# Kernel tuning notes

Measured on AMD Instinct MI355X. Metric: run time of the kernel, lower is better.

Reference implementation:

```python
import jax, jax.numpy as jnp
import numpy as np

V, D, H, L, DFF = 32000, 512, 8, 6, 2048
B, T = 64, 256
PAD_IDX = 1


def _pos_encoding(t, d):
    pos = jnp.arange(t, dtype=jnp.float32)[:, None]          # [t,1]
    i2 = jnp.arange(0, d, 2, dtype=jnp.float32)              # [d/2]
    ang = pos / jnp.power(10000.0, i2 / d)                   # [t,d/2]
    pe = jnp.zeros((t, d), dtype=jnp.float32)
    pe = pe.at[:, 0::2].set(jnp.sin(ang))
    pe = pe.at[:, 1::2].set(jnp.cos(ang))
    return pe


def _ln(x, g, b):
    mu = x.mean(-1, keepdims=True)
    var = ((x - mu) ** 2).mean(-1, keepdims=True)
    return (x - mu) * jax.lax.rsqrt(var + 1e-5) * g + b


def _mha(xq, xkv, Wq, Wk, Wv, Wo, bo, causal):
    b, tq, d = xq.shape
    tk = xkv.shape[1]
    hd = d // H
    q = (xq @ Wq).reshape(b, tq, H, hd)
    k = (xkv @ Wk).reshape(b, tk, H, hd)
    v = (xkv @ Wv).reshape(b, tk, H, hd)
    wei = jnp.einsum('bqhd,bkhd->bhqk', q, k) * (hd ** -0.5)
    if causal:
        mask = jnp.tril(jnp.ones((tq, tk), dtype=bool))
        wei = jnp.where(mask, wei, -jnp.inf)
    wei = jax.nn.softmax(wei, axis=-1)
    out = jnp.einsum('bhqk,bkhd->bqhd', wei, v).reshape(b, tq, d)
    return out @ Wo + bo


def _ffn(x, W1, b1, W2, b2):
    return jax.nn.relu(x @ W1 + b1) @ W2 + b2


def setup_inputs() -> dict:
    key = jax.random.key(0)
    ks = iter(jax.random.split(key, 64))
    nrm = lambda shape: (jax.random.normal(next(ks), shape, dtype=jnp.float32) * 0.02)
    inp = {
        'idx': jax.random.randint(next(ks), (B, T), 0, V),
        'idx_enc': jax.random.randint(next(ks), (B, T), 0, V),
        'targets': jax.random.randint(next(ks), (B, T), 0, V),
        'emb_dec': nrm((V, D)),
        'emb_enc': nrm((V, D)),
        # encoder stacks [L, ...]
        'enc_Wq': nrm((L, D, D)), 'enc_Wk': nrm((L, D, D)), 'enc_Wv': nrm((L, D, D)),
        'enc_Wo': nrm((L, D, D)), 'enc_bo': jnp.zeros((L, D)),
        'enc_ln_g': jnp.ones((L, 2, D)), 'enc_ln_b': jnp.zeros((L, 2, D)),
        'enc_W1': nrm((L, D, DFF)), 'enc_b1': jnp.zeros((L, DFF)),
        'enc_W2': nrm((L, DFF, D)), 'enc_b2': jnp.zeros((L, D)),
        # decoder stacks [L, ...]
        'dec_Wq_sa': nrm((L, D, D)), 'dec_Wk_sa': nrm((L, D, D)), 'dec_Wv_sa': nrm((L, D, D)),
        'dec_Wo_sa': nrm((L, D, D)), 'dec_bo_sa': jnp.zeros((L, D)),
        'dec_Wq_xa': nrm((L, D, D)), 'dec_Wk_xa': nrm((L, D, D)), 'dec_Wv_xa': nrm((L, D, D)),
        'dec_Wo_xa': nrm((L, D, D)), 'dec_bo_xa': jnp.zeros((L, D)),
        'dec_ln_g': jnp.ones((L, 4, D)), 'dec_ln_b': jnp.zeros((L, 4, D)),
        'dec_W1': nrm((L, D, DFF)), 'dec_b1': jnp.zeros((L, DFF)),
        'dec_W2': nrm((L, DFF, D)), 'dec_b2': jnp.zeros((L, D)),
        'lnf_g': jnp.ones((D,)), 'lnf_b': jnp.zeros((D,)),
        'Wlm': nrm((D, V)), 'blm': jnp.zeros((V,)),
    }
    return inp


def reference(idx, idx_enc, targets, emb_dec, emb_enc,
              enc_Wq, enc_Wk, enc_Wv, enc_Wo, enc_bo, enc_ln_g, enc_ln_b,
              enc_W1, enc_b1, enc_W2, enc_b2,
              dec_Wq_sa, dec_Wk_sa, dec_Wv_sa, dec_Wo_sa, dec_bo_sa,
              dec_Wq_xa, dec_Wk_xa, dec_Wv_xa, dec_Wo_xa, dec_bo_xa,
              dec_ln_g, dec_ln_b, dec_W1, dec_b1, dec_W2, dec_b2,
              lnf_g, lnf_b, Wlm, blm):
    t_dec = idx.shape[1]
    t_enc = idx_enc.shape[1]
    pe = _pos_encoding(256, D)
    # encoder
    y = emb_enc[idx_enc] + pe[:t_enc]
    for l in range(L):
        h = _ln(y, enc_ln_g[l, 0], enc_ln_b[l, 0])
        y = y + _mha(h, h, enc_Wq[l], enc_Wk[l], enc_Wv[l], enc_Wo[l], enc_bo[l], causal=False)
        h = _ln(y, enc_ln_g[l, 1], enc_ln_b[l, 1])
        y = y + _ffn(h, enc_W1[l], enc_b1[l], enc_W2[l], enc_b2[l])
    # decoder
    x = emb_dec[idx] + pe[:t_dec]
    for l in range(L):
        h = _ln(x, dec_ln_g[l, 0], dec_ln_b[l, 0])
        x = x + _mha(h, h, dec_Wq_sa[l], dec_Wk_sa[l], dec_Wv_sa[l], dec_Wo_sa[l], dec_bo_sa[l], causal=True)
        hq = _ln(x, dec_ln_g[l, 1], dec_ln_b[l, 1])
        hk = _ln(y, dec_ln_g[l, 2], dec_ln_b[l, 2])
        x = x + _mha(hq, hk, dec_Wq_xa[l], dec_Wk_xa[l], dec_Wv_xa[l], dec_Wo_xa[l], dec_bo_xa[l], causal=False)
        h = _ln(x, dec_ln_g[l, 3], dec_ln_b[l, 3])
        x = x + _ffn(h, dec_W1[l], dec_b1[l], dec_W2[l], dec_b2[l])
    x = _ln(x, lnf_g, lnf_b)
    logits = (x @ Wlm + blm).reshape(-1, V)  # [B*T, V]
    # cross entropy with ignore_index = PAD_IDX, mean over non-ignored
    tgt = targets.reshape(-1)
    logp = jax.nn.log_softmax(logits, axis=-1)
    nll = -jnp.take_along_axis(logp, tgt[:, None], axis=-1)[:, 0]
    valid = (tgt != PAD_IDX).astype(logits.dtype)
    loss = jnp.sum(nll * valid) / jnp.maximum(jnp.sum(valid), 1.0)
    return logits, loss
```

## Files before the change

### kernel.cpp

```cpp
#include <hip/hip_runtime.h>

typedef __attribute__((ext_vector_type(8))) short s8v;
typedef __attribute__((ext_vector_type(4))) float f4v;
using u16 = unsigned short;

__device__ __forceinline__ u16 f2bf(float f) {
  union { float f; unsigned u; } v; v.f = f;
  return (u16)((v.u + 0x7FFFu + ((v.u >> 16) & 1u)) >> 16);
}

__global__ __launch_bounds__(256) void pe_kernel(float* __restrict__ pe) {
  int i = blockIdx.x * 256 + threadIdx.x;
  int t = i >> 8, p = i & 255;
  float ex = (2.f * (float)p) / 512.f;
  float ang = (float)t * expf(-ex * 9.210340371976184f);
  pe[t * 512 + 2 * p]     = sinf(ang);
  pe[t * 512 + 2 * p + 1] = cosf(ang);
}

__global__ __launch_bounds__(256) void wconv_kernel(const float* __restrict__ in,
    u16* __restrict__ out, int R, int C, size_t dstride) {
  __shared__ float tile[64][65];
  const size_t mat = (size_t)R * C;
  const float* src = in + (size_t)blockIdx.z * mat;
  u16* dst = out + (size_t)blockIdx.z * dstride;
  int r0 = blockIdx.x * 64, c0 = blockIdx.y * 64;
  int tr = threadIdx.x >> 6, tc = threadIdx.x & 63;
#pragma unroll
  for (int i = 0; i < 16; ++i)
    tile[i * 4 + tr][tc] = src[(size_t)(r0 + i * 4 + tr) * C + (c0 + tc)];
  __syncthreads();
#pragma unroll
  for (int i = 0; i < 16; ++i)
    dst[(size_t)(c0 + i * 4 + tr) * R + (r0 + tc)] = f2bf(tile[tc][i * 4 + tr]);
}

__global__ __launch_bounds__(256) void embed_kernel(const int* __restrict__ idx,
    const float* __restrict__ emb, const float* __restrict__ pe, float* __restrict__ y) {
  int i = blockIdx.x * 256 + threadIdx.x;
  int row = i >> 7, c = (i & 127) * 4;
  int t = row & 255;
  int tok = idx[row];
  f4v e = *(const f4v*)(emb + (size_t)tok * 512 + c);
  f4v p = *(const f4v*)(pe + (size_t)t * 512 + c);
  *(f4v*)(y + (size_t)row * 512 + c) = e + p;
}

__global__ __launch_bounds__(256) void ln_kernel(const float* __restrict__ x,
    const float* __restrict__ g, const float* __restrict__ b, u16* __restrict__ out) {
  int row = blockIdx.x * 4 + (threadIdx.x >> 6);
  int lane = threadIdx.x & 63;
  const float* xr = x + (size_t)row * 512 + lane * 8;
  f4v v0 = *(const f4v*)xr;
  f4v v1 = *(const f4v*)(xr + 4);
  float s = v0[0] + v0[1] + v0[2] + v0[3] + v1[0] + v1[1] + v1[2] + v1[3];
#pragma unroll
  for (int o = 1; o < 64; o <<= 1) s += __shfl_xor(s, o);
  float mu = s * (1.f / 512.f);
  float q = 0.f;
#pragma unroll
  for (int j = 0; j < 4; ++j) {
    float d0 = v0[j] - mu; q += d0 * d0;
    float d1 = v1[j] - mu; q += d1 * d1;
  }
#pragma unroll
  for (int o = 1; o < 64; o <<= 1) q += __shfl_xor(q, o);
  float rs = rsqrtf(q * (1.f / 512.f) + 1e-5f);
  f4v g0 = *(const f4v*)(g + lane * 8), g1 = *(const f4v*)(g + lane * 8 + 4);
  f4v b0 = *(const f4v*)(b + lane * 8), b1 = *(const f4v*)(b + lane * 8 + 4);
  s8v ov;
#pragma unroll
  for (int j = 0; j < 4; ++j) {
    ov[j]     = (short)f2bf((v0[j] - mu) * rs * g0[j] + b0[j]);
    ov[4 + j] = (short)f2bf((v1[j] - mu) * rs * g1[j] + b1[j]);
  }
  *(s8v*)(out + (size_t)row * 512 + lane * 8) = ov;
}

template<int HAS_BIAS, int ADD_RES, int RELU, int OUT_BF16, int WLOSS, int NT, int SWZM>
__global__ __launch_bounds__(256, 4) void gemm128(
    const u16* __restrict__ A, const u16* __restrict__ Bt,
    const float* __restrict__ bias, const float* __restrict__ res,
    void* __restrict__ outp, int M, int N, int K,
    float* __restrict__ pmax, float* __restrict__ psum) {
  __shared__ __align__(16) u16 smem[2 * 128 * 64];
  u16* As = smem;
  u16* Bs = smem + 128 * 64;
  const int tid = threadIdx.x, lane = tid & 63, w = tid >> 6;
  int bx, by;
  if (SWZM == 1) {
    int flat = blockIdx.y * gridDim.x + blockIdx.x;
    int xcd = flat & 7, local = flat >> 3;
    int p = local / gridDim.y;
    by = local - p * gridDim.y;
    bx = xcd * (gridDim.x >> 3) + p;
  } else {
    int nx = gridDim.x;
    int flat = blockIdx.y * nx + blockIdx.x;
    int per = (nx * gridDim.y) >> 3;
    int sw = (flat & 7) * per + (flat >> 3);
    by = sw / nx; bx = sw - by * nx;
  }
  const int m0 = bx * 128, n0 = by * 128;
  const int wm = (w >> 1) * 64, wn = (w & 1) * 64;
  const int lhi = lane >> 4, llo = lane & 15;
  const int srow = tid >> 3;
  const int sl = tid & 7;
  const int gcol = (sl ^ (srow & 7)) * 8;

  const u16* Ag = A + (size_t)(m0 + srow) * K + gcol;
  const u16* Bg = Bt + (size_t)(n0 + srow) * K + gcol;
  const size_t rstep = (size_t)32 * K;
  const int sx = llo & 7;

  f4v acc[4][4] = {};
  const int nk = K >> 6;
  for (int t = 0; t < nk; ++t) {
    const int kt = t * 64;
#pragma unroll
    for (int q = 0; q < 4; ++q)
      __builtin_amdgcn_global_load_lds(
          (const __attribute__((address_space(1))) void*)(Ag + q * rstep + kt),
          (__attribute__((address_space(3))) void*)(&As[(q * 32 + srow) * 64 + sl * 8]),
          16, 0, 0);
#pragma unroll
    for (int q = 0; q < 4; ++q)
      __builtin_amdgcn_global_load_lds(
          (const __attribute__((address_space(1))) void*)(Bg + q * rstep + kt),
          (__attribute__((address_space(3))) void*)(&Bs[(q * 32 + srow) * 64 + sl * 8]),
          16, 0, 0);
    __syncthreads();
#pragma unroll
    for (int kk = 0; kk < 2; ++kk) {
      s8v af[4], bfv[4];
#pragma unroll
      for (int i = 0; i < 4; ++i)
        af[i] = *(const s8v*)&As[(wm + i * 16 + llo) * 64 + (((kk * 4 + lhi) ^ sx) * 8)];
#pragma unroll
      for (int j = 0; j < 4; ++j)
        bfv[j] = *(const s8v*)&Bs[(wn + j * 16 + llo) * 64 + (((kk * 4 + lhi) ^ sx) * 8)];
#pragma unroll
      for (int i = 0; i < 4; ++i)
#pragma unroll
        for (int j = 0; j < 4; ++j)
          acc[i][j] = __builtin_amdgcn_mfma_f32_16x16x32_bf16(af[i], bfv[j], acc[i][j], 0, 0, 0);
    }
    __syncthreads();
  }

  if (OUT_BF16) {
    float bvj[4];
#pragma unroll
    for (int j = 0; j < 4; ++j)
      bvj[j] = HAS_BIAS ? bias[n0 + wn + j * 16 + llo] : 0.f;
#pragma unroll
    for (int i = 0; i < 4; ++i) {
#pragma unroll
      for (int j = 0; j < 4; ++j) {
        int col = n0 + wn + j * 16 + llo;
#pragma unroll
        for (int r = 0; r < 4; ++r) {
          int row = m0 + wm + i * 16 + lhi * 4 + r;
          float v = acc[i][j][r] + bvj[j];
          if (RELU) v = fmaxf(v, 0.f);
          ((u16*)outp)[(size_t)row * N + col] = f2bf(v);
        }
      }
    }
  } else {
    float* lb = (float*)smem;
    float* wbuf = lb + w * 1088;
    float* lbm = lb + 4608;
    float* lbs = lb + 4864;
    f4v bias4 = {0.f, 0.f, 0.f, 0.f};
    if (HAS_BIAS) bias4 = *(const f4v*)(bias + n0 + wn + llo * 4);
#pragma unroll
    for (int i = 0; i < 4; ++i) {
#pragma unroll
      for (int j = 0; j < 4; ++j)
#pragma unroll
        for (int r = 0; r < 4; ++r)
          wbuf[(lhi * 4 + r) * 68 + j * 16 + llo] = acc[i][j][r];
      asm volatile("s_waitcnt lgkmcnt(0)" ::: "memory");
      __builtin_amdgcn_sched_barrier(0);
#pragma unroll
      for (int p = 0; p < 4; ++p) {
        int r16 = p * 4 + lhi;
        f4v v4 = *(const f4v*)&wbuf[r16 * 68 + llo * 4];
        v4 += bias4;
        int grow = m0 + wm + i * 16 + r16;
        int gcol4 = n0 + wn + llo * 4;
        if (ADD_RES) v4 += *(const f4v*)(res + (size_t)grow * N + gcol4);
        if (RELU) {
          v4[0] = fmaxf(v4[0], 0.f); v4[1] = fmaxf(v4[1], 0.f);
          v4[2] = fmaxf(v4[2], 0.f); v4[3] = fmaxf(v4[3], 0.f);
        }
        float* dst = (float*)outp + (size_t)grow * N + gcol4;
        if (NT) __builtin_nontemporal_store(v4, (f4v*)dst);
        else    *(f4v*)dst = v4;
        if (WLOSS) {
          float mx = fmaxf(fmaxf(v4[0], v4[1]), fmaxf(v4[2], v4[3]));
          mx = fmaxf(mx, __shfl_xor(mx, 1));
          mx = fmaxf(mx, __shfl_xor(mx, 2));
          mx = fmaxf(mx, __shfl_xor(mx, 4));
          mx = fmaxf(mx, __shfl_xor(mx, 8));
          float sum = __expf(v4[0] - mx) + __expf(v4[1] - mx)
                    + __expf(v4[2] - mx) + __expf(v4[3] - mx);
          sum += __shfl_xor(sum, 1); sum += __shfl_xor(sum, 2);
          sum += __shfl_xor(sum, 4); sum += __shfl_xor(sum, 8);
          if (llo == 0) {
            int lr = wm + i * 16 + r16;
            lbm[lr * 2 + (wn >> 6)] = mx;
            lbs[lr * 2 + (wn >> 6)] = sum;
          }
        }
      }
      asm volatile("s_waitcnt lgkmcnt(0)" ::: "memory");
      __builtin_amdgcn_sched_barrier(0);
    }
    if (WLOSS) {
      __syncthreads();
      if (tid < 128) {
        float ma = lbm[tid * 2], mb = lbm[tid * 2 + 1];
        float sa = lbs[tid * 2], sb = lbs[tid * 2 + 1];
        float m = fmaxf(ma, mb);
        float ss = sa * __expf(ma - m) + sb * __expf(mb - m);
        int ntile = N >> 7;
        pmax[(size_t)(m0 + tid) * ntile + by] = m;
        psum[(size_t)(m0 + tid) * ntile + by] = ss;
      }
    }
  }
}

__global__ __launch_bounds__(256) void attn_kernel(
    const u16* __restrict__ Qp, int qs, const u16* __restrict__ Kp,
    const u16* __restrict__ Vp, int kvs, u16* __restrict__ Ob, int causal) {
  __shared__ __align__(16) u16 Ks[256][72];
  __shared__ __align__(16) u16 Vt[64][264];
  __shared__ __align__(16) u16 Ps[4][16][264];
  const int tid = threadIdx.x, lane = tid & 63, w = tid >> 6;
  const int b = blockIdx.x >> 3, h = blockIdx.x & 7;
  const size_t qbase  = (size_t)b * 256 * qs  + (size_t)h * 64;
  const size_t kvbase = (size_t)b * 256 * kvs + (size_t)h * 64;
  const size_t obase  = (size_t)b * 256 * 512 + (size_t)h * 64;
  {
    int t0 = tid >> 3, d0 = (tid & 7) * 8;
#pragma unroll
    for (int it = 0; it < 8; ++it) {
      int t = it * 32 + t0;
      s8v kv = *(const s8v*)(Kp + kvbase + (size_t)t * kvs + d0);
      *(s8v*)&Ks[t][d0] = kv;
      s8v vv = *(const s8v*)(Vp + kvbase + (size_t)t * kvs + d0);
#pragma unroll
      for (int j = 0; j < 8; ++j) Vt[d0 + j][t] = (u16)vv[j];
    }
  }
  __syncthreads();
  const int lhi = lane >> 4, llo = lane & 15;
  for (int qc = 0; qc < 4; ++qc) {
    const int qr0 = w * 64 + qc * 16;
    s8v aq0 = *(const s8v*)(Qp + qbase + (size_t)(qr0 + llo) * qs + lhi * 8);
    s8v aq1 = *(const s8v*)(Qp + qbase + (size_t)(qr0 + llo) * qs + 32 + lhi * 8);
    f4v S[16];
#pragma unroll
    for (int c = 0; c < 16; ++c) {
      s8v bk0 = *(const s8v*)&Ks[c * 16 + llo][lhi * 8];
      s8v bk1 = *(const s8v*)&Ks[c * 16 + llo][32 + lhi * 8];
      f4v z = {0.f, 0.f, 0.f, 0.f};
      z = __builtin_amdgcn_mfma_f32_16x16x32_bf16(aq0, bk0, z, 0, 0, 0);
      S[c] = __builtin_amdgcn_mfma_f32_16x16x32_bf16(aq1, bk1, z, 0, 0, 0);
    }
#pragma unroll
    for (int r = 0; r < 4; ++r) {
      const int tq = qr0 + lhi * 4 + r;
      float mx = -1e30f;
#pragma unroll
      for (int c = 0; c < 16; ++c) {
        float s = S[c][r] * 0.125f;
        if (causal && (c * 16 + llo) > tq) s = -1e30f;
        S[c][r] = s;
        mx = fmaxf(mx, s);
      }
      mx = fmaxf(mx, __shfl_xor(mx, 1));
      mx = fmaxf(mx, __shfl_xor(mx, 2));
      mx = fmaxf(mx, __shfl_xor(mx, 4));
      mx = fmaxf(mx, __shfl_xor(mx, 8));
      float sum = 0.f;
#pragma unroll
      for (int c = 0; c < 16; ++c) { float p = __expf(S[c][r] - mx); S[c][r] = p; sum += p; }
      sum += __shfl_xor(sum, 1); sum += __shfl_xor(sum, 2);
      sum += __shfl_xor(sum, 4); sum += __shfl_xor(sum, 8);
      float inv = 1.f / sum;
#pragma unroll
      for (int c = 0; c < 16; ++c)
        Ps[w][lhi * 4 + r][c * 16 + llo] = f2bf(S[c][r] * inv);
    }
    asm volatile("s_waitcnt lgkmcnt(0)" ::: "memory");
    f4v o[4] = {};
#pragma unroll
    for (int kb = 0; kb < 8; ++kb) {
      s8v pa = *(const s8v*)&Ps[w][llo][kb * 32 + lhi * 8];
#pragma unroll
      for (int nb = 0; nb < 4; ++nb) {
        s8v bv = *(const s8v*)&Vt[nb * 16 + llo][kb * 32 + lhi * 8];
        o[nb] = __builtin_amdgcn_mfma_f32_16x16x32_bf16(pa, bv, o[nb], 0, 0, 0);
      }
    }
#pragma unroll
    for (int nb = 0; nb < 4; ++nb)
#pragma unroll
      for (int r = 0; r < 4; ++r)
        Ob[obase + (size_t)(qr0 + lhi * 4 + r) * 512 + nb * 16 + llo] = f2bf(o[nb][r]);
  }
}

__global__ __launch_bounds__(256) void loss_lse_kernel(const float* __restrict__ pmax,
    const float* __restrict__ psum, const float* __restrict__ logits,
    const int* __restrict__ tgt, float* __restrict__ nll, float* __restrict__ valid) {
  const int w = threadIdx.x >> 6, lane = threadIdx.x & 63;
  const int row = blockIdx.x * 4 + w;
  float m = -1e30f, s = 0.f;
  for (int e = lane; e < 250; e += 64) {
    float pm = pmax[(size_t)row * 250 + e], ps = psum[(size_t)row * 250 + e];
    if (pm > m) { s = s * __expf(m - pm) + ps; m = pm; }
    else          s += ps * __expf(pm - m);
  }
#pragma unroll
  for (int o = 1; o < 64; o <<= 1) {
    float om = __shfl_xor(m, o), os = __shfl_xor(s, o);
    float mm = fmaxf(m, om);
    s = s * __expf(m - mm) + os * __expf(om - mm);
    m = mm;
  }
  if (lane == 0) {
    int t = tgt[row];
    float lse = m + logf(s);
    float v = (t != 1) ? 1.f : 0.f;
    nll[row] = v * (lse - logits[(size_t)row * 32000 + t]);
    valid[row] = v;
  }
}

__global__ __launch_bounds__(256) void loss_final_kernel(const float* __restrict__ nll,
    const float* __restrict__ valid, float* __restrict__ out) {
  __shared__ float sa[256], sb[256];
  int tid = threadIdx.x;
  float s = 0.f, c = 0.f;
  for (int i = tid; i < 16384; i += 256) { s += nll[i]; c += valid[i]; }
  sa[tid] = s; sb[tid] = c;
  __syncthreads();
  for (int st = 128; st > 0; st >>= 1) {
    if (tid < st) { sa[tid] += sa[tid + st]; sb[tid] += sb[tid + st]; }
    __syncthreads();
  }
  if (tid == 0) out[0] = sa[0] / fmaxf(sb[0], 1.f);
}

extern "C" void kernel_launch(void* const* d_in, const int* in_sizes, int n_in,
                              void* d_out, int out_size, void* d_ws, size_t ws_size,
                              hipStream_t stream) {
  (void)in_sizes; (void)n_in; (void)out_size; (void)ws_size;
  const int* idx       = (const int*)d_in[0];
  const int* idx_enc   = (const int*)d_in[1];
  const int* targets   = (const int*)d_in[2];
  const float* emb_dec = (const float*)d_in[3];
  const float* emb_enc = (const float*)d_in[4];
  const float* enc_Wq  = (const float*)d_in[5];
  const float* enc_Wk  = (const float*)d_in[6];
  const float* enc_Wv  = (const float*)d_in[7];
  const float* enc_Wo  = (const float*)d_in[8];
  const float* enc_bo  = (const float*)d_in[9];
  const float* enc_ln_g = (const float*)d_in[10];
  const float* enc_ln_b = (const float*)d_in[11];
  const float* enc_W1  = (const float*)d_in[12];
  const float* enc_b1  = (const float*)d_in[13];
  const float* enc_W2  = (const float*)d_in[14];
  const float* enc_b2  = (const float*)d_in[15];
  const float* dWq_sa  = (const float*)d_in[16];
  const float* dWk_sa  = (const float*)d_in[17];
  const float* dWv_sa  = (const float*)d_in[18];
  const float* dWo_sa  = (const float*)d_in[19];
  const float* dbo_sa  = (const float*)d_in[20];
  const float* dWq_xa  = (const float*)d_in[21];
  const float* dWk_xa  = (const float*)d_in[22];
  const float* dWv_xa  = (const float*)d_in[23];
  const float* dWo_xa  = (const float*)d_in[24];
  const float* dbo_xa  = (const float*)d_in[25];
  const float* dec_ln_g = (const float*)d_in[26];
  const float* dec_ln_b = (const float*)d_in[27];
  const float* dec_W1  = (const float*)d_in[28];
  const float* dec_b1  = (const float*)d_in[29];
  const float* dec_W2  = (const float*)d_in[30];
  const float* dec_b2  = (const float*)d_in[31];
  const float* lnf_g   = (const float*)d_in[32];
  const float* lnf_b   = (const float*)d_in[33];
  const float* Wlm     = (const float*)d_in[34];
  const float* blm     = (const float*)d_in[35];
  float* out_logits = (float*)d_out;
  float* out_loss   = out_logits + (size_t)16384 * 32000;

  size_t off = 0;
  auto alloc = [&](size_t bytes) -> char* {
    char* p = (char*)d_ws + off;
    off += (bytes + 255) & ~(size_t)255;
    return p;
  };
  const size_t SQ = 512 * 512, SF = 512 * 2048;
  u16* tWqkvE = (u16*)alloc(6 * 3 * SQ * 2);
  u16* tWoE   = (u16*)alloc(6 * SQ * 2);
  u16* tW1E   = (u16*)alloc(6 * SF * 2);
  u16* tW2E   = (u16*)alloc(6 * SF * 2);
  u16* tWqkvS = (u16*)alloc(6 * 3 * SQ * 2);
  u16* tWoS   = (u16*)alloc(6 * SQ * 2);
  u16* tWqX   = (u16*)alloc(6 * SQ * 2);
  u16* tWkvX  = (u16*)alloc(6 * 2 * SQ * 2);
  u16* tWoX   = (u16*)alloc(6 * SQ * 2);
  u16* tW1D   = (u16*)alloc(6 * SF * 2);
  u16* tW2D   = (u16*)alloc(6 * SF * 2);
  u16* tWlm   = (u16*)alloc((size_t)32000 * 512 * 2);
  float* pe   = (float*)alloc(256 * 512 * 4);
  float* yE   = (float*)alloc((size_t)16384 * 512 * 4);
  float* xD   = (float*)alloc((size_t)16384 * 512 * 4);
  u16* hA     = (u16*)alloc((size_t)16384 * 512 * 2);
  u16* hB     = (u16*)alloc((size_t)16384 * 512 * 2);
  u16* qkvB   = (u16*)alloc((size_t)16384 * 1536 * 2);
  u16* qB     = (u16*)alloc((size_t)16384 * 512 * 2);
  u16* kvB    = (u16*)alloc((size_t)16384 * 1024 * 2);
  u16* atB    = (u16*)alloc((size_t)16384 * 512 * 2);
  u16* midB   = (u16*)alloc((size_t)16384 * 2048 * 2);
  float* pmax = (float*)alloc((size_t)16384 * 250 * 4);
  float* psum = (float*)alloc((size_t)16384 * 250 * 4);
  float* rnll = (float*)alloc(16384 * 4);
  float* rval = (float*)alloc(16384 * 4);

  dim3 tb(256);
  const size_t S3 = 3 * SQ, S2 = 2 * SQ;
  wconv_kernel<<<dim3(8, 8, 6), tb, 0, stream>>>(enc_Wq, tWqkvE + 0 * SQ, 512, 512, S3);
  wconv_kernel<<<dim3(8, 8, 6), tb, 0, stream>>>(enc_Wk, tWqkvE + 1 * SQ, 512, 512, S3);
  wconv_kernel<<<dim3(8, 8, 6), tb, 0, stream>>>(enc_Wv, tWqkvE + 2 * SQ, 512, 512, S3);
  wconv_kernel<<<dim3(8, 8, 6), tb, 0, stream>>>(enc_Wo, tWoE, 512, 512, SQ);
  wconv_kernel<<<dim3(8, 32, 6), tb, 0, stream>>>(enc_W1, tW1E, 512, 2048, SF);
  wconv_kernel<<<dim3(32, 8, 6), tb, 0, stream>>>(enc_W2, tW2E, 2048, 512, SF);
  wconv_kernel<<<dim3(8, 8, 6), tb, 0, stream>>>(dWq_sa, tWqkvS + 0 * SQ, 512, 512, S3);
  wconv_kernel<<<dim3(8, 8, 6), tb, 0, stream>>>(dWk_sa, tWqkvS + 1 * SQ, 512, 512, S3);
  wconv_kernel<<<dim3(8, 8, 6), tb, 0, stream>>>(dWv_sa, tWqkvS + 2 * SQ, 512, 512, S3);
  wconv_kernel<<<dim3(8, 8, 6), tb, 0, stream>>>(dWo_sa, tWoS, 512, 512, SQ);
  wconv_kernel<<<dim3(8, 8, 6), tb, 0, stream>>>(dWq_xa, tWqX, 512, 512, SQ);
  wconv_kernel<<<dim3(8, 8, 6), tb, 0, stream>>>(dWk_xa, tWkvX + 0 * SQ, 512, 512, S2);
  wconv_kernel<<<dim3(8, 8, 6), tb, 0, stream>>>(dWv_xa, tWkvX + 1 * SQ, 512, 512, S2);
  wconv_kernel<<<dim3(8, 8, 6), tb, 0, stream>>>(dWo_xa, tWoX, 512, 512, SQ);
  wconv_kernel<<<dim3(8, 32, 6), tb, 0, stream>>>(dec_W1, tW1D, 512, 2048, SF);
  wconv_kernel<<<dim3(32, 8, 6), tb, 0, stream>>>(dec_W2, tW2D, 2048, 512, SF);
  wconv_kernel<<<dim3(8, 500, 1), tb, 0, stream>>>(Wlm, tWlm, 512, 32000, (size_t)0);
  pe_kernel<<<256, 256, 0, stream>>>(pe);

  auto ln = [&](const float* xin, const float* g, const float* bb, u16* o) {
    ln_kernel<<<4096, 256, 0, stream>>>(xin, g, bb, o);
  };
  auto g_bf16 = [&](const u16* Ap, const u16* Bp, u16* Op, int N) {
    gemm128<0, 0, 0, 1, 0, 0, 0><<<dim3(128, N / 128), 256, 0, stream>>>(
        Ap, Bp, nullptr, nullptr, Op, 16384, N, 512, nullptr, nullptr);
  };
  auto proj_res = [&](const u16* Ap, const u16* Bp, const float* bi, float* xr, int K) {
    gemm128<1, 1, 0, 0, 0, 0, 0><<<dim3(128, 4), 256, 0, stream>>>(
        Ap, Bp, bi, xr, xr, 16384, 512, K, nullptr, nullptr);
  };
  auto ffn1 = [&](const u16* Ap, const u16* Bp, const float* bi, u16* Op) {
    gemm128<1, 0, 1, 1, 0, 0, 0><<<dim3(128, 16), 256, 0, stream>>>(
        Ap, Bp, bi, nullptr, Op, 16384, 2048, 512, nullptr, nullptr);
  };

  embed_kernel<<<8192, 256, 0, stream>>>(idx_enc, emb_enc, pe, yE);
  for (int l = 0; l < 6; ++l) {
    ln(yE, enc_ln_g + (l * 2 + 0) * 512, enc_ln_b + (l * 2 + 0) * 512, hA);
    g_bf16(hA, tWqkvE + l * S3, qkvB, 1536);
    attn_kernel<<<512, 256, 0, stream>>>(qkvB, 1536, qkvB + 512, qkvB + 1024, 1536, atB, 0);
    proj_res(atB, tWoE + l * SQ, enc_bo + l * 512, yE, 512);
    ln(yE, enc_ln_g + (l * 2 + 1) * 512, enc_ln_b + (l * 2 + 1) * 512, hA);
    ffn1(hA, tW1E + l * SF, enc_b1 + l * 2048, midB);
    proj_res(midB, tW2E + l * SF, enc_b2 + l * 512, yE, 2048);
  }

  embed_kernel<<<8192, 256, 0, stream>>>(idx, emb_dec, pe, xD);
  for (int l = 0; l < 6; ++l) {
    ln(xD, dec_ln_g + (l * 4 + 0) * 512, dec_ln_b + (l * 4 + 0) * 512, hA);
    g_bf16(hA, tWqkvS + l * S3, qkvB, 1536);
    attn_kernel<<<512, 256, 0, stream>>>(qkvB, 1536, qkvB + 512, qkvB + 1024, 1536, atB, 1);
    proj_res(atB, tWoS + l * SQ, dbo_sa + l * 512, xD, 512);
    ln(xD, dec_ln_g + (l * 4 + 1) * 512, dec_ln_b + (l * 4 + 1) * 512, hA);
    ln(yE, dec_ln_g + (l * 4 + 2) * 512, dec_ln_b + (l * 4 + 2) * 512, hB);
    g_bf16(hA, tWqX + l * SQ, qB, 512);
    g_bf16(hB, tWkvX + l * S2, kvB, 1024);
    attn_kernel<<<512, 256, 0, stream>>>(qB, 512, kvB, kvB + 512, 1024, atB, 0);
    proj_res(atB, tWoX + l * SQ, dbo_xa + l * 512, xD, 512);
    ln(xD, dec_ln_g + (l * 4 + 3) * 512, dec_ln_b + (l * 4 + 3) * 512, hA);
    ffn1(hA, tW1D + l * SF, dec_b1 + l * 2048, midB);
    proj_res(midB, tW2D + l * SF, dec_b2 + l * 512, xD, 2048);
  }

  ln(xD, lnf_g, lnf_b, hA);
  gemm128<1, 0, 0, 0, 1, 1, 1><<<dim3(128, 250), 256, 0, stream>>>(
      hA, tWlm, blm, nullptr, out_logits, 16384, 32000, 512, pmax, psum);
  loss_lse_kernel<<<4096, 256, 0, stream>>>(pmax, psum, out_logits, targets, rnll, rval);
  loss_final_kernel<<<1, 256, 0, stream>>>(rnll, rval, out_loss);
}
```

Before: 4.918 ms.

## Rewrite attention as flash-style KV tiling and fuse LN, embedding, cross-attn GEMMs

Attention now walks K/V in four 64-row tiles with an online softmax, keeping Q fragments in registers, skipping fully masked causal tiles, and using much less shared memory so two blocks can share a CU. Embedding is fused with the first layernorm, the two cross-attention layernorms are merged into one launch, and the Q and KV projections run as one dual-operand GEMM launch. The twelve square weight conversions are batched into a single kernel. These cut launches and extra activation passes, but the tiled attention adds more barriers and rescaling work per tile.

Result: no change. 4.836 ms (-1.7%).

```diff
diff --git a/kernel.cpp b/kernel.cpp
--- a/kernel.cpp
+++ b/kernel.cpp
@@ -35,15 +35,47 @@
     dst[(size_t)(c0 + i * 4 + tr) * R + (r0 + tc)] = f2bf(tile[tc][i * 4 + tr]);
 }
 
-__global__ __launch_bounds__(256) void embed_kernel(const int* __restrict__ idx,
-    const float* __restrict__ emb, const float* __restrict__ pe, float* __restrict__ y) {
-  int i = blockIdx.x * 256 + threadIdx.x;
-  int row = i >> 7, c = (i & 127) * 4;
-  int t = row & 255;
-  int tok = idx[row];
-  f4v e = *(const f4v*)(emb + (size_t)tok * 512 + c);
-  f4v p = *(const f4v*)(pe + (size_t)t * 512 + c);
-  *(f4v*)(y + (size_t)row * 512 + c) = e + p;
+struct WcSq { const float* src[12]; u16* dst[12]; unsigned long long dstr[12]; };
+__global__ __launch_bounds__(256) void wconv_sq_kernel(WcSq S) {
+  __shared__ float tile[64][65];
+  int mm = blockIdx.z / 6, l = blockIdx.z % 6;
+  const float* src = S.src[mm] + (size_t)l * 512 * 512;
+  u16* dst = S.dst[mm] + (size_t)l * S.dstr[mm];
+  int r0 = blockIdx.x * 64, c0 = blockIdx.y * 64;
+  int tr = threadIdx.x >> 6, tc = threadIdx.x & 63;
+#pragma unroll
+  for (int i = 0; i < 16; ++i)
+    tile[i * 4 + tr][tc] = src[(size_t)(r0 + i * 4 + tr) * 512 + (c0 + tc)];
+  __syncthreads();
+#pragma unroll
+  for (int i = 0; i < 16; ++i)
+    dst[(size_t)(c0 + i * 4 + tr) * 512 + (r0 + tc)] = f2bf(tile[tc][i * 4 + tr]);
+}
+
+__device__ __forceinline__ void ln_row(f4v v0, f4v v1, const float* g, const float* b,
+                                       int lane, u16* outrow) {
+  float s = v0[0] + v0[1] + v0[2] + v0[3] + v1[0] + v1[1] + v1[2] + v1[3];
+#pragma unroll
+  for (int o = 1; o < 64; o <<= 1) s += __shfl_xor(s, o);
+  float mu = s * (1.f / 512.f);
+  float q = 0.f;
+#pragma unroll
+  for (int j = 0; j < 4; ++j) {
+    float d0 = v0[j] - mu; q += d0 * d0;
+    float d1 = v1[j] - mu; q += d1 * d1;
+  }
+#pragma unroll
+  for (int o = 1; o < 64; o <<= 1) q += __shfl_xor(q, o);
+  float rs = rsqrtf(q * (1.f / 512.f) + 1e-5f);
+  f4v g0 = *(const f4v*)(g + lane * 8), g1 = *(const f4v*)(g + lane * 8 + 4);
+  f4v b0 = *(const f4v*)(b + lane * 8), b1 = *(const f4v*)(b + lane * 8 + 4);
+  s8v ov;
+#pragma unroll
+  for (int j = 0; j < 4; ++j) {
+    ov[j]     = (short)f2bf((v0[j] - mu) * rs * g0[j] + b0[j]);
+    ov[4 + j] = (short)f2bf((v1[j] - mu) * rs * g1[j] + b1[j]);
+  }
+  *(s8v*)(outrow + lane * 8) = ov;
 }
 
 __global__ __launch_bounds__(256) void ln_kernel(const float* __restrict__ x,
@@ -51,38 +83,46 @@
   int row = blockIdx.x * 4 + (threadIdx.x >> 6);
   int lane = threadIdx.x & 63;
   const float* xr = x + (size_t)row * 512 + lane * 8;
-  f4v v0 = *(const f4v*)xr;
-  f4v v1 = *(const f4v*)(xr + 4);
-  float s = v0[0] + v0[1] + v0[2] + v0[3] + v1[0] + v1[1] + v1[2] + v1[3];
-#pragma unroll
-  for (int o = 1; o < 64; o <<= 1) s += __shfl_xor(s, o);
-  float mu = s * (1.f / 512.f);
-  float q = 0.f;
-#pragma unroll
-  for (int j = 0; j < 4; ++j) {
-    float d0 = v0[j] - mu; q += d0 * d0;
-    float d1 = v1[j] - mu; q += d1 * d1;
-  }
-#pragma unroll
-  for (int o = 1; o < 64; o <<= 1) q += __shfl_xor(q, o);
-  float rs = rsqrtf(q * (1.f / 512.f) + 1e-5f);
-  f4v g0 = *(const f4v*)(g + lane * 8), g1 = *(const f4v*)(g + lane * 8 + 4);
-  f4v b0 = *(const f4v*)(b + lane * 8), b1 = *(const f4v*)(b + lane * 8 + 4);
-  s8v ov;
-#pragma unroll
-  for (int j = 0; j < 4; ++j) {
-    ov[j]     = (short)f2bf((v0[j] - mu) * rs * g0[j] + b0[j]);
-    ov[4 + j] = (short)f2bf((v1[j] - mu) * rs * g1[j] + b1[j]);
-  }
-  *(s8v*)(out + (size_t)row * 512 + lane * 8) = ov;
-}
-
-template<int HAS_BIAS, int ADD_RES, int RELU, int OUT_BF16, int WLOSS, int NT, int SWZM>
+  ln_row(*(const f4v*)xr, *(const f4v*)(xr + 4), g, b, lane, out + (size_t)row * 512);
+}
+
+__global__ __launch_bounds__(256) void ln2_kernel(
+    const float* __restrict__ x1, const float* __restrict__ g1, const float* __restrict__ b1,
+    u16* __restrict__ o1, const float* __restrict__ x2, const float* __restrict__ g2,
+    const float* __restrict__ b2, u16* __restrict__ o2) {
+  int row = blockIdx.x * 4 + (threadIdx.x >> 6);
+  int lane = threadIdx.x & 63;
+  const float* x = x1; const float* g = g1; const float* b = b1; u16* o = o1;
+  if (row >= 16384) { row -= 16384; x = x2; g = g2; b = b2; o = o2; }
+  const float* xr = x + (size_t)row * 512 + lane * 8;
+  ln_row(*(const f4v*)xr, *(const f4v*)(xr + 4), g, b, lane, o + (size_t)row * 512);
+}
+
+__global__ __launch_bounds__(256) void emb_ln_kernel(const int* __restrict__ idx,
+    const float* __restrict__ emb, const float* __restrict__ pe,
+    const float* __restrict__ g, const float* __restrict__ b,
+    float* __restrict__ y, u16* __restrict__ h) {
+  int row = blockIdx.x * 4 + (threadIdx.x >> 6);
+  int lane = threadIdx.x & 63;
+  int tok = idx[row], t = row & 255;
+  const float* e = emb + (size_t)tok * 512 + lane * 8;
+  const float* p = pe + (size_t)t * 512 + lane * 8;
+  f4v v0 = *(const f4v*)e + *(const f4v*)p;
+  f4v v1 = *(const f4v*)(e + 4) + *(const f4v*)(p + 4);
+  float* yr = y + (size_t)row * 512 + lane * 8;
+  *(f4v*)yr = v0; *(f4v*)(yr + 4) = v1;
+  ln_row(v0, v1, g, b, lane, h + (size_t)row * 512);
+}
+
+template<int HAS_BIAS, int ADD_RES, int RELU, int OUT_BF16, int WLOSS, int NT,
+         int SWZM, int DUAL>
 __global__ __launch_bounds__(256, 4) void gemm128(
     const u16* __restrict__ A, const u16* __restrict__ Bt,
     const float* __restrict__ bias, const float* __restrict__ res,
     void* __restrict__ outp, int M, int N, int K,
-    float* __restrict__ pmax, float* __restrict__ psum) {
+    float* __restrict__ pmax, float* __restrict__ psum,
+    const u16* __restrict__ A2, const u16* __restrict__ Bt2,
+    void* __restrict__ out2) {
   __shared__ __align__(16) u16 smem[2 * 128 * 64];
   u16* As = smem;
   u16* Bs = smem + 128 * 64;
@@ -101,6 +141,7 @@
     int sw = (flat & 7) * per + (flat >> 3);
     by = sw / nx; bx = sw - by * nx;
   }
+  if (DUAL && by >= 4) { A = A2; Bt = Bt2; outp = out2; N = 1024; by -= 4; }
   const int m0 = bx * 128, n0 = by * 128;
   const int wm = (w >> 1) * 64, wn = (w & 1) * 64;
   const int lhi = lane >> 4, llo = lane & 15;
@@ -233,86 +274,117 @@
   }
 }
 
-__global__ __launch_bounds__(256) void attn_kernel(
+__global__ __launch_bounds__(256, 2) void attn_kernel(
     const u16* __restrict__ Qp, int qs, const u16* __restrict__ Kp,
     const u16* __restrict__ Vp, int kvs, u16* __restrict__ Ob, int causal) {
-  __shared__ __align__(16) u16 Ks[256][72];
-  __shared__ __align__(16) u16 Vt[64][264];
-  __shared__ __align__(16) u16 Ps[4][16][264];
+  __shared__ __align__(16) u16 Ks[64][72];
+  __shared__ __align__(16) u16 Vt[64][66];
+  __shared__ __align__(16) u16 Ps[4][16][66];
   const int tid = threadIdx.x, lane = tid & 63, w = tid >> 6;
   const int b = blockIdx.x >> 3, h = blockIdx.x & 7;
   const size_t qbase  = (size_t)b * 256 * qs  + (size_t)h * 64;
   const size_t kvbase = (size_t)b * 256 * kvs + (size_t)h * 64;
   const size_t obase  = (size_t)b * 256 * 512 + (size_t)h * 64;
-  {
-    int t0 = tid >> 3, d0 = (tid & 7) * 8;
-#pragma unroll
-    for (int it = 0; it < 8; ++it) {
-      int t = it * 32 + t0;
-      s8v kv = *(const s8v*)(Kp + kvbase + (size_t)t * kvs + d0);
-      *(s8v*)&Ks[t][d0] = kv;
-      s8v vv = *(const s8v*)(Vp + kvbase + (size_t)t * kvs + d0);
-#pragma unroll
-      for (int j = 0; j < 8; ++j) Vt[d0 + j][t] = (u16)vv[j];
+  const int lhi = lane >> 4, llo = lane & 15;
+  s8v aq0[4], aq1[4];
+#pragma unroll
+  for (int qc = 0; qc < 4; ++qc) {
+    const u16* qp = Qp + qbase + (size_t)(w * 64 + qc * 16 + llo) * qs;
+    aq0[qc] = *(const s8v*)(qp + lhi * 8);
+    aq1[qc] = *(const s8v*)(qp + 32 + lhi * 8);
+  }
+  f4v o[4][4] = {};
+  float mrow[16], lrow[16];
+#pragma unroll
+  for (int i = 0; i < 16; ++i) { mrow[i] = -1e30f; lrow[i] = 0.f; }
+
+  for (int kt = 0; kt < 4; ++kt) {
+    if (kt) __syncthreads();
+    {
+      int tr = tid >> 3, d0 = (tid & 7) * 8;
+#pragma unroll
+      for (int it = 0; it < 2; ++it) {
+        int t = it * 32 + tr;
+        const u16* kp = Kp + kvbase + (size_t)(kt * 64 + t) * kvs + d0;
+        *(s8v*)&Ks[t][d0] = *(const s8v*)kp;
+        s8v vv = *(const s8v*)(Vp + kvbase + (size_t)(kt * 64 + t) * kvs + d0);
+#pragma unroll
+        for (int j = 0; j < 8; ++j) Vt[d0 + j][t] = (u16)vv[j];
+      }
     }
-  }
-  __syncthreads();
-  const int lhi = lane >> 4, llo = lane & 15;
-  for (int qc = 0; qc < 4; ++qc) {
-    const int qr0 = w * 64 + qc * 16;
-    s8v aq0 = *(const s8v*)(Qp + qbase + (size_t)(qr0 + llo) * qs + lhi * 8);
-    s8v aq1 = *(const s8v*)(Qp + qbase + (size_t)(qr0 + llo) * qs + 32 + lhi * 8);
-    f4v S[16];
-#pragma unroll
-    for (int c = 0; c < 16; ++c) {
-      s8v bk0 = *(const s8v*)&Ks[c * 16 + llo][lhi * 8];
-      s8v bk1 = *(const s8v*)&Ks[c * 16 + llo][32 + lhi * 8];
-      f4v z = {0.f, 0.f, 0.f, 0.f};
-      z = __builtin_amdgcn_mfma_f32_16x16x32_bf16(aq0, bk0, z, 0, 0, 0);
-      S[c] = __builtin_amdgcn_mfma_f32_16x16x32_bf16(aq1, bk1, z, 0, 0, 0);
+    __syncthreads();
+#pragma unroll
+    for (int qc = 0; qc < 4; ++qc) {
+      if (causal && kt * 64 > w * 64 + qc * 16 + 15) continue;
+      f4v S[4];
+#pragma unroll
+      for (int c = 0; c < 4; ++c) {
+        s8v bk0 = *(const s8v*)&Ks[c * 16 + llo][lhi * 8];
+        s8v bk1 = *(const s8v*)&Ks[c * 16 + llo][32 + lhi * 8];
+        f4v z = {0.f, 0.f, 0.f, 0.f};
+        z = __builtin_amdgcn_mfma_f32_16x16x32_bf16(aq0[qc], bk0, z, 0, 0, 0);
+        S[c] = __builtin_amdgcn_mfma_f32_16x16x32_bf16(aq1[qc], bk1, z, 0, 0, 0);
+      }
+      float scv[4];
+#pragma unroll
+      for (int r = 0; r < 4; ++r) {
+        const int tq = w * 64 + qc * 16 + lhi * 4 + r;
+        float tmax = -1e30f;
+#pragma unroll
+        for (int c = 0; c < 4; ++c) {
+          float s = S[c][r] * 0.125f;
+          if (causal && (kt * 64 + c * 16 + llo) > tq) s = -1e30f;
+          S[c][r] = s;
+          tmax = fmaxf(tmax, s);
+        }
+        tmax = fmaxf(tmax, __shfl_xor(tmax, 1));
+        tmax = fmaxf(tmax, __shfl_xor(tmax, 2));
+        tmax = fmaxf(tmax, __shfl_xor(tmax, 4));
+        tmax = fmaxf(tmax, __shfl_xor(tmax, 8));
+        float mo = mrow[qc * 4 + r];
+        float mn = fmaxf(mo, tmax);
+        float sc = __expf(mo - mn);
+        float sum = 0.f;
+#pragma unroll
+        for (int c = 0; c < 4; ++c) {
+          float p = __expf(S[c][r] - mn);
+          sum += p;
+          Ps[w][lhi * 4 + r][c * 16 + llo] = f2bf(p);
+        }
+        sum += __shfl_xor(sum, 1); sum += __shfl_xor(sum, 2);
+        sum += __shfl_xor(sum, 4); sum += __shfl_xor(sum, 8);
+        lrow[qc * 4 + r] = lrow[qc * 4 + r] * sc + sum;
+        mrow[qc * 4 + r] = mn;
+        scv[r] = sc;
+      }
+#pragma unroll
+      for (int nb = 0; nb < 4; ++nb)
+#pragma unroll
+        for (int r = 0; r < 4; ++r)
+          o[qc][nb][r] *= scv[r];
+      asm volatile("s_waitcnt lgkmcnt(0)" ::: "memory");
+      __builtin_amdgcn_sched_barrier(0);
+#pragma unroll
+      for (int kb = 0; kb < 2; ++kb) {
+        s8v pa = *(const s8v*)&Ps[w][llo][kb * 32 + lhi * 8];
+#pragma unroll
+        for (int nb = 0; nb < 4; ++nb) {
+          s8v bv = *(const s8v*)&Vt[nb * 16 + llo][kb * 32 + lhi * 8];
+          o[qc][nb] = __builtin_amdgcn_mfma_f32_16x16x32_bf16(pa, bv, o[qc][nb], 0, 0, 0);
+        }
+      }
     }
-#pragma unroll
-    for (int r = 0; r < 4; ++r) {
-      const int tq = qr0 + lhi * 4 + r;
-      float mx = -1e30f;
-#pragma unroll
-      for (int c = 0; c < 16; ++c) {
-        float s = S[c][r] * 0.125f;
-        if (causal && (c * 16 + llo) > tq) s = -1e30f;
-        S[c][r] = s;
-        mx = fmaxf(mx, s);
-      }
-      mx = fmaxf(mx, __shfl_xor(mx, 1));
-      mx = fmaxf(mx, __shfl_xor(mx, 2));
-      mx = fmaxf(mx, __shfl_xor(mx, 4));
-      mx = fmaxf(mx, __shfl_xor(mx, 8));
-      float sum = 0.f;
-#pragma unroll
-      for (int c = 0; c < 16; ++c) { float p = __expf(S[c][r] - mx); S[c][r] = p; sum += p; }
-      sum += __shfl_xor(sum, 1); sum += __shfl_xor(sum, 2);
-      sum += __shfl_xor(sum, 4); sum += __shfl_xor(sum, 8);
-      float inv = 1.f / sum;
-#pragma unroll
-      for (int c = 0; c < 16; ++c)
-        Ps[w][lhi * 4 + r][c * 16 + llo] = f2bf(S[c][r] * inv);
-    }
-    asm volatile("s_waitcnt lgkmcnt(0)" ::: "memory");
-    f4v o[4] = {};
-#pragma unroll
-    for (int kb = 0; kb < 8; ++kb) {
-      s8v pa = *(const s8v*)&Ps[w][llo][kb * 32 + lhi * 8];
-#pragma unroll
-      for (int nb = 0; nb < 4; ++nb) {
-        s8v bv = *(const s8v*)&Vt[nb * 16 + llo][kb * 32 + lhi * 8];
-        o[nb] = __builtin_amdgcn_mfma_f32_16x16x32_bf16(pa, bv, o[nb], 0, 0, 0);
-      }
-    }
+  }
+#pragma unroll
+  for (int qc = 0; qc < 4; ++qc)
 #pragma unroll
     for (int nb = 0; nb < 4; ++nb)
 #pragma unroll
-      for (int r = 0; r < 4; ++r)
-        Ob[obase + (size_t)(qr0 + lhi * 4 + r) * 512 + nb * 16 + llo] = f2bf(o[nb][r]);
-  }
+      for (int r = 0; r < 4; ++r) {
+        float inv = 1.f / lrow[qc * 4 + r];
+        Ob[obase + (size_t)(w * 64 + qc * 16 + lhi * 4 + r) * 512 + nb * 16 + llo] =
+            f2bf(o[qc][nb][r] * inv);
+      }
 }
 
 __global__ __launch_bounds__(256) void loss_lse_kernel(const float* __restrict__ pmax,
@@ -436,20 +508,24 @@
 
   dim3 tb(256);
   const size_t S3 = 3 * SQ, S2 = 2 * SQ;
-  wconv_kernel<<<dim3(8, 8, 6), tb, 0, stream>>>(enc_Wq, tWqkvE + 0 * SQ, 512, 512, S3);
-  wconv_kernel<<<dim3(8, 8, 6), tb, 0, stream>>>(enc_Wk, tWqkvE + 1 * SQ, 512, 512, S3);
-  wconv_kernel<<<dim3(8, 8, 6), tb, 0, stream>>>(enc_Wv, tWqkvE + 2 * SQ, 512, 512, S3);
-  wconv_kernel<<<dim3(8, 8, 6), tb, 0, stream>>>(enc_Wo, tWoE, 512, 512, SQ);
+  {
+    WcSq S;
+    S.src[0] = enc_Wq;  S.dst[0] = tWqkvE + 0 * SQ; S.dstr[0] = S3;
+    S.src[1] = enc_Wk;  S.dst[1] = tWqkvE + 1 * SQ; S.dstr[1] = S3;
+    S.src[2] = enc_Wv;  S.dst[2] = tWqkvE + 2 * SQ; S.dstr[2] = S3;
+    S.src[3] = enc_Wo;  S.dst[3] = tWoE;            S.dstr[3] = SQ;
+    S.src[4] = dWq_sa;  S.dst[4] = tWqkvS + 0 * SQ; S.dstr[4] = S3;
+    S.src[5] = dWk_sa;  S.dst[5] = tWqkvS + 1 * SQ; S.dstr[5] = S3;
+    S.src[6] = dWv_sa;  S.dst[6] = tWqkvS + 2 * SQ; S.dstr[6] = S3;
+    S.src[7] = dWo_sa;  S.dst[7] = tWoS;            S.dstr[7] = SQ;
+    S.src[8] = dWq_xa;  S.dst[8] = tWqX;            S.dstr[8] = SQ;
+    S.src[9] = dWk_xa;  S.dst[9] = tWkvX + 0 * SQ;  S.dstr[9] = S2;
+    S.src[10] = dWv_xa; S.dst[10] = tWkvX + 1 * SQ; S.dstr[10] = S2;
+    S.src[11] = dWo_xa; S.dst[11] = tWoX;           S.dstr[11] = SQ;
+    wconv_sq_kernel<<<dim3(8, 8, 72), tb, 0, stream>>>(S);
+  }
   wconv_kernel<<<dim3(8, 32, 6), tb, 0, stream>>>(enc_W1, tW1E, 512, 2048, SF);
   wconv_kernel<<<dim3(32, 8, 6), tb, 0, stream>>>(enc_W2, tW2E, 2048, 512, SF);
-  wconv_kernel<<<dim3(8, 8, 6), tb, 0, stream>>>(dWq_sa, tWqkvS + 0 * SQ, 512, 512, S3);
-  wconv_kernel<<<dim3(8, 8, 6), tb, 0, stream>>>(dWk_sa, tWqkvS + 1 * SQ, 512, 512, S3);
-  wconv_kernel<<<dim3(8, 8, 6), tb, 0, stream>>>(dWv_sa, tWqkvS + 2 * SQ, 512, 512, S3);
-  wconv_kernel<<<dim3(8, 8, 6), tb, 0, stream>>>(dWo_sa, tWoS, 512, 512, SQ);
-  wconv_kernel<<<dim3(8, 8, 6), tb, 0, stream>>>(dWq_xa, tWqX, 512, 512, SQ);
-  wconv_kernel<<<dim3(8, 8, 6), tb, 0, stream>>>(dWk_xa, tWkvX + 0 * SQ, 512, 512, S2);
-  wconv_kernel<<<dim3(8, 8, 6), tb, 0, stream>>>(dWv_xa, tWkvX + 1 * SQ, 512, 512, S2);
-  wconv_kernel<<<dim3(8, 8, 6), tb, 0, stream>>>(dWo_xa, tWoX, 512, 512, SQ);
   wconv_kernel<<<dim3(8, 32, 6), tb, 0, stream>>>(dec_W1, tW1D, 512, 2048, SF);
   wconv_kernel<<<dim3(32, 8, 6), tb, 0, stream>>>(dec_W2, tW2D, 2048, 512, SF);
   wconv_kernel<<<dim3(8, 500, 1), tb, 0, stream>>>(Wlm, tWlm, 512, 32000, (size_t)0);
@@ -459,21 +535,31 @@
     ln_kernel<<<4096, 256, 0, stream>>>(xin, g, bb, o);
   };
   auto g_bf16 = [&](const u16* Ap, const u16* Bp, u16* Op, int N) {
-    gemm128<0, 0, 0, 1, 0, 0, 0><<<dim3(128, N / 128), 256, 0, stream>>>(
-        Ap, Bp, nullptr, nullptr, Op, 16384, N, 512, nullptr, nullptr);
+    gemm128<0, 0, 0, 1, 0, 0, 0, 0><<<dim3(128, N / 128), 256, 0, stream>>>(
+        Ap, Bp, nullptr, nullptr, Op, 16384, N, 512, nullptr, nullptr,
+        nullptr, nullptr, nullptr);
+  };
+  auto g_qkv_x = [&](const u16* Aq, const u16* Bq, u16* Oq,
+                     const u16* Akv, const u16* Bkv, u16* Okv) {
+    gemm128<0, 0, 0, 1, 0, 0, 0, 1><<<dim3(128, 12), 256, 0, stream>>>(
+        Aq, Bq, nullptr, nullptr, Oq, 16384, 512, 512, nullptr, nullptr,
+        Akv, Bkv, Okv);
   };
   auto proj_res = [&](const u16* Ap, const u16* Bp, const float* bi, float* xr, int K) {
-    gemm128<1, 1, 0, 0, 0, 0, 0><<<dim3(128, 4), 256, 0, stream>>>(
-        Ap, Bp, bi, xr, xr, 16384, 512, K, nullptr, nullptr);
+    gemm128<1, 1, 0, 0, 0, 0, 0, 0><<<dim3(128, 4), 256, 0, stream>>>(
+        Ap, Bp, bi, xr, xr, 16384, 512, K, nullptr, nullptr,
+        nullptr, nullptr, nullptr);
   };
   auto ffn1 = [&](const u16* Ap, const u16* Bp, const float* bi, u16* Op) {
-    gemm128<1, 0, 1, 1, 0, 0, 0><<<dim3(128, 16), 256, 0, stream>>>(
-        Ap, Bp, bi, nullptr, Op, 16384, 2048, 512, nullptr, nullptr);
+    gemm128<1, 0, 1, 1, 0, 0, 0, 0><<<dim3(128, 16), 256, 0, stream>>>(
+        Ap, Bp, bi, nullptr, Op, 16384, 2048, 512, nullptr, nullptr,
+        nullptr, nullptr, nullptr);
   };
 
-  embed_kernel<<<8192, 256, 0, stream>>>(idx_enc, emb_enc, pe, yE);
+  emb_ln_kernel<<<4096, 256, 0, stream>>>(idx_enc, emb_enc, pe,
+      enc_ln_g + 0, enc_ln_b + 0, yE, hA);
   for (int l = 0; l < 6; ++l) {
-    ln(yE, enc_ln_g + (l * 2 + 0) * 512, enc_ln_b + (l * 2 + 0) * 512, hA);
+    if (l) ln(yE, enc_ln_g + (l * 2 + 0) * 512, enc_ln_b + (l * 2 + 0) * 512, hA);
     g_bf16(hA, tWqkvE + l * S3, qkvB, 1536);
     attn_kernel<<<512, 256, 0, stream>>>(qkvB, 1536, qkvB + 512, qkvB + 1024, 1536, atB, 0);
     proj_res(atB, tWoE + l * SQ, enc_bo + l * 512, yE, 512);
@@ -482,16 +568,17 @@
     proj_res(midB, tW2E + l * SF, enc_b2 + l * 512, yE, 2048);
   }
 
-  embed_kernel<<<8192, 256, 0, stream>>>(idx, emb_dec, pe, xD);
+  emb_ln_kernel<<<4096, 256, 0, stream>>>(idx, emb_dec, pe,
+      dec_ln_g + 0, dec_ln_b + 0, xD, hA);
   for (int l = 0; l < 6; ++l) {
-    ln(xD, dec_ln_g + (l * 4 + 0) * 512, dec_ln_b + (l * 4 + 0) * 512, hA);
+    if (l) ln(xD, dec_ln_g + (l * 4 + 0) * 512, dec_ln_b + (l * 4 + 0) * 512, hA);
     g_bf16(hA, tWqkvS + l * S3, qkvB, 1536);
     attn_kernel<<<512, 256, 0, stream>>>(qkvB, 1536, qkvB + 512, qkvB + 1024, 1536, atB, 1);
     proj_res(atB, tWoS + l * SQ, dbo_sa + l * 512, xD, 512);
-    ln(xD, dec_ln_g + (l * 4 + 1) * 512, dec_ln_b + (l * 4 + 1) * 512, hA);
-    ln(yE, dec_ln_g + (l * 4 + 2) * 512, dec_ln_b + (l * 4 + 2) * 512, hB);
-    g_bf16(hA, tWqX + l * SQ, qB, 512);
-    g_bf16(hB, tWkvX + l * S2, kvB, 1024);
+    ln2_kernel<<<8192, 256, 0, stream>>>(
+        xD, dec_ln_g + (l * 4 + 1) * 512, dec_ln_b + (l * 4 + 1) * 512, hA,
+        yE, dec_ln_g + (l * 4 + 2) * 512, dec_ln_b + (l * 4 + 2) * 512, hB);
+    g_qkv_x(hA, tWqX + l * SQ, qB, hB, tWkvX + l * S2, kvB);
     attn_kernel<<<512, 256, 0, stream>>>(qB, 512, kvB, kvB + 512, 1024, atB, 0);
     proj_res(atB, tWoX + l * SQ, dbo_xa + l * 512, xD, 512);
     ln(xD, dec_ln_g + (l * 4 + 3) * 512, dec_ln_b + (l * 4 + 3) * 512, hA);
@@ -500,8 +587,9 @@
   }
 
   ln(xD, lnf_g, lnf_b, hA);
-  gemm128<1, 0, 0, 0, 1, 1, 1><<<dim3(128, 250), 256, 0, stream>>>(
-      hA, tWlm, blm, nullptr, out_logits, 16384, 32000, 512, pmax, psum);
+  gemm128<1, 0, 0, 0, 1, 1, 1, 0><<<dim3(128, 250), 256, 0, stream>>>(
+      hA, tWlm, blm, nullptr, out_logits, 16384, 32000, 512, pmax, psum,
+      nullptr, nullptr, nullptr);
   loss_lse_kernel<<<4096, 256, 0, stream>>>(pmax, psum, out_logits, targets, rnll, rval);
   loss_final_kernel<<<1, 256, 0, stream>>>(rnll, rval, out_loss);
 }
```
